# Kernel optimization log

Hardware: AMD Instinct MI355X
Metric: run time of the kernel (lower is better)

## Reference

```python
import jax, jax.numpy as jnp
import numpy as np

N_NODES = 100000
N_EDGES = 1600000
F_IN, F_HID, F_OUT = 48, 16, 16
K = 2  # kernel_size, dim=1, degree=1 open B-spline -> basis (1-u, u)


def glorot(key, shape):
    fan_in, fan_out = shape[-2], shape[-1]
    s = jnp.sqrt(6.0 / (fan_in + fan_out))
    return jax.random.uniform(key, shape, jnp.float32, -s, s)


def setup_inputs() -> dict:
    key = jax.random.key(0)
    ks = jax.random.split(key, 10)
    x = jax.random.normal(ks[0], (N_NODES, F_IN), jnp.float32)
    edge_attr = jax.random.uniform(ks[1], (N_EDGES, 1), jnp.float32)
    edge_index = jax.random.randint(ks[2], (2, N_EDGES), 0, N_NODES, jnp.int64)
    W1 = glorot(ks[3], (K, F_IN, F_HID))
    root1 = glorot(ks[4], (F_IN, F_HID))
    b1 = jnp.zeros((F_HID,), jnp.float32)
    W2 = glorot(ks[5], (K, F_HID, F_OUT))
    root2 = glorot(ks[6], (F_HID, F_OUT))
    b2 = jnp.zeros((F_OUT,), jnp.float32)
    return {"x": x, "edge_attr": edge_attr, "edge_index": edge_index,
            "W1": W1, "root1": root1, "b1": b1, "W2": W2, "root2": root2, "b2": b2}


def spline_conv(x, edge_index, u, W, root, bias, num_nodes):
    # x: [N,Fin], u: [E] pseudo coords in [0,1], W: [2,Fin,Fout]
    src, dst = edge_index[0], edge_index[1]
    xj = x[src]                                        # [E,Fin] gather
    m = jnp.einsum('ef,kfo->eko', xj, W)               # [E,2,Fout]
    basis = jnp.stack([1.0 - u, u], axis=1)            # linear open B-spline, K=2
    msg = jnp.einsum('ek,eko->eo', basis, m)           # [E,Fout]
    agg = jax.ops.segment_sum(msg, dst, num_segments=num_nodes)
    cnt = jax.ops.segment_sum(jnp.ones_like(msg[:, 0]), dst, num_segments=num_nodes)
    agg = agg / jnp.maximum(cnt, 1.0)[:, None]         # aggr='mean'
    return agg + x @ root + bias                       # root_weight + bias


def reference(x, edge_attr, edge_index, W1, root1, b1, W2, root2, b2):
    u = edge_attr[:, 0]
    h = jax.nn.elu(spline_conv(x, edge_index, u, W1, root1, b1, N_NODES))
    out = spline_conv(h, edge_index, u, W2, root2, b2, N_NODES)
    return jax.nn.log_softmax(out, axis=1)
```

## Files before the change

### kernel.cpp

```cpp
#include <hip/hip_runtime.h>
#include <math.h>

#define N_NODES 100000
#define N_EDGES 1600000
#define NBUK 782
#define BNODES 128
#define CAPSH 12
#define CAP 4096
#define NCHUNK 256
#define CPE 6250
#define NTBLK 1563
#define WS 52

#define NTL(p) __builtin_nontemporal_load(p)

__device__ __forceinline__ unsigned bf16_rne(float x) {
    unsigned u = __float_as_uint(x);
    return (u + 0x7FFFu + ((u >> 16) & 1u)) >> 16;
}

__device__ __forceinline__ void acc4(float* acc, uint4 w, float uu) {
    acc[0] += fmaf(uu, __uint_as_float(w.x & 0xFFFF0000u), __uint_as_float(w.x << 16));
    acc[1] += fmaf(uu, __uint_as_float(w.y & 0xFFFF0000u), __uint_as_float(w.y << 16));
    acc[2] += fmaf(uu, __uint_as_float(w.z & 0xFFFF0000u), __uint_as_float(w.z << 16));
    acc[3] += fmaf(uu, __uint_as_float(w.w & 0xFFFF0000u), __uint_as_float(w.w << 16));
}

__device__ __forceinline__ void edge_accum(unsigned pk,
                                           const uint4* __restrict__ YPH,
                                           float acc[16]) {
    float uu = (float)(pk >> 17) * (1.0f / 32767.0f);
    const uint4* yp = YPH + (size_t)(pk & 0x1FFFFu) * 4;
    uint4 w0 = yp[0], w1 = yp[1], w2 = yp[2], w3 = yp[3];
    acc4(acc + 0, w0, uu);
    acc4(acc + 4, w1, uu);
    acc4(acc + 8, w2, uu);
    acc4(acc + 12, w3, uu);
}

__device__ __forceinline__ void edge_accum2(unsigned p0, unsigned p1,
                                            const uint4* __restrict__ YPH,
                                            float acc[16]) {
    float u0 = (float)(p0 >> 17) * (1.0f / 32767.0f);
    float u1 = (float)(p1 >> 17) * (1.0f / 32767.0f);
    const uint4* a = YPH + (size_t)(p0 & 0x1FFFFu) * 4;
    const uint4* b = YPH + (size_t)(p1 & 0x1FFFFu) * 4;
    uint4 w0 = a[0], w1 = a[1], w2 = a[2], w3 = a[3];
    uint4 v0 = b[0], v1 = b[1], v2 = b[2], v3 = b[3];
    acc4(acc + 0, w0, u0);
    acc4(acc + 4, w1, u0);
    acc4(acc + 8, w2, u0);
    acc4(acc + 12, w3, u0);
    acc4(acc + 0, v0, u1);
    acc4(acc + 4, v1, u1);
    acc4(acc + 8, v2, u1);
    acc4(acc + 12, v3, u1);
}

__global__ __launch_bounds__(1024)
void transform1(const float* __restrict__ X,
                const float* __restrict__ W,
                const float* __restrict__ root,
                const float* __restrict__ bias,
                unsigned* __restrict__ YPH, float* __restrict__ R,
                int* __restrict__ cursor) {
    int t = threadIdx.x;
    if (blockIdx.x == NTBLK) {
        if (t < NBUK) cursor[t] = t * CAP;
        return;
    }
    __shared__ float sW0[16 * WS];
    __shared__ float sWd[16 * WS];
    __shared__ float sR[16 * WS];
    __shared__ float sB[16];
    for (int i = t; i < 48 * 16; i += 1024) {
        int f = i >> 4, o = i & 15;
        float w0 = W[i];
        float w1 = W[48 * 16 + i];
        sW0[o * WS + f] = w0;
        sWd[o * WS + f] = w1 - w0;
        sR[o * WS + f]  = root[i];
    }
    if (t < 16) sB[t] = bias[t];
    __syncthreads();

    int idx = blockIdx.x * 1024 + t;
    int n = idx >> 4;
    int o = idx & 15;
    if (n >= N_NODES) return;

    const float4* xr  = (const float4*)(X + (long)n * 48);
    const float4* w0p = (const float4*)(sW0 + o * WS);
    const float4* wdp = (const float4*)(sWd + o * WS);
    const float4* wrp = (const float4*)(sR  + o * WS);
    float a0 = 0.0f, a1 = 0.0f, ar = 0.0f;
#pragma unroll
    for (int fc = 0; fc < 12; ++fc) {
        float4 xv = xr[fc];
        float4 w0 = w0p[fc];
        float4 wd = wdp[fc];
        float4 wr = wrp[fc];
        a0 = fmaf(xv.x, w0.x, a0); a0 = fmaf(xv.y, w0.y, a0);
        a0 = fmaf(xv.z, w0.z, a0); a0 = fmaf(xv.w, w0.w, a0);
        a1 = fmaf(xv.x, wd.x, a1); a1 = fmaf(xv.y, wd.y, a1);
        a1 = fmaf(xv.z, wd.z, a1); a1 = fmaf(xv.w, wd.w, a1);
        ar = fmaf(xv.x, wr.x, ar); ar = fmaf(xv.y, wr.y, ar);
        ar = fmaf(xv.z, wr.z, ar); ar = fmaf(xv.w, wr.w, ar);
    }
    YPH[idx] = bf16_rne(a0) | (bf16_rne(a1) << 16);
    R[idx]   = ar + sB[o];
}

__global__ __launch_bounds__(1024)
void scatter_edges(const int* __restrict__ src, const int* __restrict__ dst,
                   const float* __restrict__ u,
                   int* __restrict__ cursor,
                   unsigned* __restrict__ pkb, unsigned char* __restrict__ dlb) {
    __shared__ unsigned upk[CPE];
    __shared__ unsigned short ubuk[CPE];
    __shared__ unsigned char udl[CPE];
    __shared__ unsigned spk[CPE];
    __shared__ unsigned char sdl[CPE];
    __shared__ unsigned short sbuk[CPE];
    __shared__ int lcur[NBUK];
    __shared__ int gbase[NBUK];
    __shared__ int sc[1024];

    int t = threadIdx.x, c = blockIdx.x;

    for (int i = t; i < NBUK; i += 1024) lcur[i] = 0;
    __syncthreads();
    for (int j = t; j < CPE; j += 1024) {
        int e = c * CPE + j;
        int d = NTL(dst + e);
        float uu = NTL(u + e);
        uu = uu < 0.0f ? 0.0f : (uu > 1.0f ? 1.0f : uu);
        int u15 = (int)fmaf(uu, 32767.0f, 0.5f);
        upk[j] = (unsigned)NTL(src + e) | ((unsigned)u15 << 17);
        udl[j] = (unsigned char)(d & 127);
        int b = d >> 7;
        ubuk[j] = (unsigned short)b;
        atomicAdd(&lcur[b], 1);
    }
    __syncthreads();

    int v = (t < NBUK) ? lcur[t] : 0;
    sc[t] = v;
    __syncthreads();
    for (int off = 1; off < 1024; off <<= 1) {
        int x = (t >= off) ? sc[t - off] : 0;
        __syncthreads();
        sc[t] += x;
        __syncthreads();
    }
    if (t < NBUK) {
        int ex = sc[t] - v;
        lcur[t] = ex;
        int base = atomicAdd(&cursor[t], v);
        gbase[t] = base - ex;
    }
    __syncthreads();

    for (int j = t; j < CPE; j += 1024) {
        int b = ubuk[j];
        int p = atomicAdd(&lcur[b], 1);
        spk[p] = upk[j];
        sdl[p] = udl[j];
        sbuk[p] = (unsigned short)b;
    }
    __syncthreads();

    for (int j = t; j < CPE; j += 1024) {
        int b = sbuk[j];
        int g = gbase[b] + j;
        if (g < ((b + 1) << CAPSH)) {
            pkb[g] = spk[j];
            dlb[g] = sdl[j];
        }
    }
}

__global__ __launch_bounds__(512)
void aggregate1(const int* __restrict__ cursor,
                const unsigned* __restrict__ pkb,
                const unsigned char* __restrict__ dlb,
                const uint4* __restrict__ YPH1,
                const float* __restrict__ R1,
                const float* __restrict__ W2,
                const float* __restrict__ root2,
                const float* __restrict__ b2,
                unsigned* __restrict__ YPH2,
                float* __restrict__ R2) {
    __shared__ unsigned spk[CAP];
    __shared__ int rp[BNODES + 1];
    __shared__ int cur[BNODES];
    __shared__ float sW0[256], sWd[256], sR[256], sB[16];
    int t = threadIdx.x, b = blockIdx.x;

    if (t < 256) {
        float w0 = W2[t], w1 = W2[256 + t];
        sW0[t] = w0;
        sWd[t] = w1 - w0;
        sR[t]  = root2[t];
    }
    if (t < 16) sB[t] = b2[t];
    if (t < BNODES) cur[t] = 0;
    __syncthreads();

    int cnt = cursor[b] - (b << CAPSH);
    if (cnt > CAP) cnt = CAP;
    const unsigned* pk = pkb + ((size_t)b << CAPSH);
    const unsigned char* dl = dlb + ((size_t)b << CAPSH);

    for (int j = t; j < cnt; j += 512) atomicAdd(&cur[NTL(dl + j)], 1);
    __syncthreads();

    int v = 0;
    if (t < BNODES) { v = cur[t]; rp[t] = v; }
    __syncthreads();
    for (int off = 1; off < BNODES; off <<= 1) {
        int x = 0;
        if (t < BNODES && t >= off) x = rp[t - off];
        __syncthreads();
        if (t < BNODES) rp[t] += x;
        __syncthreads();
    }
    if (t < BNODES) { int ex = rp[t] - v; rp[t] = ex; cur[t] = ex; }
    if (t == 0) rp[BNODES] = cnt;
    __syncthreads();

    for (int j = t; j < cnt; j += 512) {
        int d = NTL(dl + j);
        unsigned p = NTL(pk + j);
        int pos = atomicAdd(&cur[d], 1);
        spk[pos] = p;
    }
    __syncthreads();

    int node = t >> 2, q = t & 3;
    int n = (b << 7) + node;
    int beg = rp[node], end = rp[node + 1];
    int deg = end - beg;

    float acc[16];
#pragma unroll
    for (int i = 0; i < 16; ++i) acc[i] = 0.0f;
    int j = beg + q;
    for (; j + 4 < end; j += 8)
        edge_accum2(spk[j], spk[j + 4], YPH1, acc);
    if (j < end) edge_accum(spk[j], YPH1, acc);

#pragma unroll
    for (int mask = 1; mask <= 2; mask <<= 1) {
#pragma unroll
        for (int i = 0; i < 16; ++i) acc[i] += __shfl_xor(acc[i], mask);
    }

    if (n < N_NODES) {
        float inv = 1.0f / (deg > 0 ? (float)deg : 1.0f);
        float h16[16];
        const float4* rrp = (const float4*)(R1 + (size_t)n * 16);
#pragma unroll
        for (int qq = 0; qq < 4; ++qq) {
            float4 rr = rrp[qq];
            float w;
            w = fmaf(acc[4 * qq + 0], inv, rr.x); h16[4 * qq + 0] = w > 0.0f ? w : expm1f(w);
            w = fmaf(acc[4 * qq + 1], inv, rr.y); h16[4 * qq + 1] = w > 0.0f ? w : expm1f(w);
            w = fmaf(acc[4 * qq + 2], inv, rr.z); h16[4 * qq + 2] = w > 0.0f ? w : expm1f(w);
            w = fmaf(acc[4 * qq + 3], inv, rr.w); h16[4 * qq + 3] = w > 0.0f ? w : expm1f(w);
        }

        float a0[4] = {0, 0, 0, 0}, a1[4] = {0, 0, 0, 0}, ar[4] = {0, 0, 0, 0};
        int o0 = q * 4;
#pragma unroll
        for (int f = 0; f < 16; ++f) {
            float hv = h16[f];
#pragma unroll
            for (int o = 0; o < 4; ++o) {
                a0[o] = fmaf(hv, sW0[f * 16 + o0 + o], a0[o]);
                a1[o] = fmaf(hv, sWd[f * 16 + o0 + o], a1[o]);
                ar[o] = fmaf(hv, sR [f * 16 + o0 + o], ar[o]);
            }
        }
        uint4 yw;
        yw.x = bf16_rne(a0[0]) | (bf16_rne(a1[0]) << 16);
        yw.y = bf16_rne(a0[1]) | (bf16_rne(a1[1]) << 16);
        yw.z = bf16_rne(a0[2]) | (bf16_rne(a1[2]) << 16);
        yw.w = bf16_rne(a0[3]) | (bf16_rne(a1[3]) << 16);
        ((uint4*)YPH2)[(size_t)n * 4 + q] = yw;
        float4 rv;
        rv.x = ar[0] + sB[o0 + 0];
        rv.y = ar[1] + sB[o0 + 1];
        rv.z = ar[2] + sB[o0 + 2];
        rv.w = ar[3] + sB[o0 + 3];
        ((float4*)R2)[(size_t)n * 4 + q] = rv;
    }
}

__global__ __launch_bounds__(512)
void aggregate2(const int* __restrict__ cursor,
                const unsigned* __restrict__ pkb,
                const unsigned char* __restrict__ dlb,
                const uint4* __restrict__ YPH2,
                const float* __restrict__ R2,
                float* __restrict__ out) {
    __shared__ unsigned spk[CAP];
    __shared__ int rp[BNODES + 1];
    __shared__ int cur[BNODES];
    int t = threadIdx.x, b = blockIdx.x;

    if (t < BNODES) cur[t] = 0;
    __syncthreads();

    int cnt = cursor[b] - (b << CAPSH);
    if (cnt > CAP) cnt = CAP;
    const unsigned* pk = pkb + ((size_t)b << CAPSH);
    const unsigned char* dl = dlb + ((size_t)b << CAPSH);

    for (int j = t; j < cnt; j += 512) atomicAdd(&cur[NTL(dl + j)], 1);
    __syncthreads();

    int v = 0;
    if (t < BNODES) { v = cur[t]; rp[t] = v; }
    __syncthreads();
    for (int off = 1; off < BNODES; off <<= 1) {
        int x = 0;
        if (t < BNODES && t >= off) x = rp[t - off];
        __syncthreads();
        if (t < BNODES) rp[t] += x;
        __syncthreads();
    }
    if (t < BNODES) { int ex = rp[t] - v; rp[t] = ex; cur[t] = ex; }
    if (t == 0) rp[BNODES] = cnt;
    __syncthreads();

    for (int j = t; j < cnt; j += 512) {
        int d = NTL(dl + j);
        unsigned p = NTL(pk + j);
        int pos = atomicAdd(&cur[d], 1);
        spk[pos] = p;
    }
    __syncthreads();

    int node = t >> 2, q = t & 3;
    int n = (b << 7) + node;
    int beg = rp[node], end = rp[node + 1];
    int deg = end - beg;

    float acc[16];
#pragma unroll
    for (int i = 0; i < 16; ++i) acc[i] = 0.0f;
    int j = beg + q;
    for (; j + 4 < end; j += 8)
        edge_accum2(spk[j], spk[j + 4], YPH2, acc);
    if (j < end) edge_accum(spk[j], YPH2, acc);

#pragma unroll
    for (int mask = 1; mask <= 2; mask <<= 1) {
#pragma unroll
        for (int i = 0; i < 16; ++i) acc[i] += __shfl_xor(acc[i], mask);
    }

    if (n < N_NODES) {
        float inv = 1.0f / (deg > 0 ? (float)deg : 1.0f);
        float4 rr = ((const float4*)R2)[(size_t)n * 4 + q];
        float v0 = fmaf(acc[4 * q + 0], inv, rr.x);
        float v1 = fmaf(acc[4 * q + 1], inv, rr.y);
        float v2 = fmaf(acc[4 * q + 2], inv, rr.z);
        float v3 = fmaf(acc[4 * q + 3], inv, rr.w);
        float m = fmaxf(fmaxf(v0, v1), fmaxf(v2, v3));
        m = fmaxf(m, __shfl_xor(m, 1));
        m = fmaxf(m, __shfl_xor(m, 2));
        float s = expf(v0 - m) + expf(v1 - m) + expf(v2 - m) + expf(v3 - m);
        s += __shfl_xor(s, 1);
        s += __shfl_xor(s, 2);
        float lse = m + logf(s);
        float4 ov = make_float4(v0 - lse, v1 - lse, v2 - lse, v3 - lse);
        ((float4*)out)[(size_t)n * 4 + q] = ov;
    }
}

extern "C" void kernel_launch(void* const* d_in, const int* in_sizes, int n_in,
                              void* d_out, int out_size, void* d_ws, size_t ws_size,
                              hipStream_t stream) {
    const float* x         = (const float*)d_in[0];
    const float* edge_attr = (const float*)d_in[1];
    const int*   edge_idx  = (const int*)d_in[2];
    const float* W1        = (const float*)d_in[3];
    const float* root1     = (const float*)d_in[4];
    const float* b1        = (const float*)d_in[5];
    const float* W2        = (const float*)d_in[6];
    const float* root2     = (const float*)d_in[7];
    const float* b2        = (const float*)d_in[8];
    float* out = (float*)d_out;

    const int* src = edge_idx;
    const int* dst = edge_idx + N_EDGES;

    char* ws = (char*)d_ws;
    unsigned*      pkb    = (unsigned*)(ws);
    unsigned char* dlb    = (unsigned char*)(ws + 12812288);
    unsigned*      YPH1   = (unsigned*)(ws + 16015360);
    float*         R1     = (float*)(ws + 22415360);
    unsigned*      YPH2   = (unsigned*)(ws + 28815360);
    float*         R2     = (float*)(ws + 35215360);
    int*           cursor = (int*)(ws + 41615360);

    transform1<<<dim3(NTBLK + 1), 1024, 0, stream>>>(
        x, W1, root1, b1, YPH1, R1, cursor);

    scatter_edges<<<dim3(NCHUNK), 1024, 0, stream>>>(
        src, dst, edge_attr, cursor, pkb, dlb);

    aggregate1<<<dim3(NBUK), 512, 0, stream>>>(
        cursor, pkb, dlb, (const uint4*)YPH1, R1, W2, root2, b2, YPH2, R2);

    aggregate2<<<dim3(NBUK), 512, 0, stream>>>(
        cursor, pkb, dlb, (const uint4*)YPH2, R2, out);
}
```

Measured before the change: 189.2 us.

## Persist sorted edge order and row pointers from layer 1 for layer 2

```diff
diff --git a/kernel.cpp b/kernel.cpp
--- a/kernel.cpp
+++ b/kernel.cpp
@@ -7,10 +7,11 @@
 #define BNODES 128
 #define CAPSH 12
 #define CAP 4096
-#define NCHUNK 256
-#define CPE 6250
+#define NCHUNK 512
+#define CPE 3125
 #define NTBLK 1563
 #define WS 52
+#define RPW (BNODES + 1)
 
 #define NTL(p) __builtin_nontemporal_load(p)
 
@@ -182,8 +183,9 @@
 
 __global__ __launch_bounds__(512)
 void aggregate1(const int* __restrict__ cursor,
-                const unsigned* __restrict__ pkb,
+                unsigned* __restrict__ pkb,
                 const unsigned char* __restrict__ dlb,
+                int* __restrict__ rptab,
                 const uint4* __restrict__ YPH1,
                 const float* __restrict__ R1,
                 const float* __restrict__ W2,
@@ -192,7 +194,7 @@
                 unsigned* __restrict__ YPH2,
                 float* __restrict__ R2) {
     __shared__ unsigned spk[CAP];
-    __shared__ int rp[BNODES + 1];
+    __shared__ int rp[RPW];
     __shared__ int cur[BNODES];
     __shared__ float sW0[256], sWd[256], sR[256], sB[16];
     int t = threadIdx.x, b = blockIdx.x;
@@ -209,10 +211,18 @@
 
     int cnt = cursor[b] - (b << CAPSH);
     if (cnt > CAP) cnt = CAP;
-    const unsigned* pk = pkb + ((size_t)b << CAPSH);
+    unsigned* pk = pkb + ((size_t)b << CAPSH);
     const unsigned char* dl = dlb + ((size_t)b << CAPSH);
-
-    for (int j = t; j < cnt; j += 512) atomicAdd(&cur[NTL(dl + j)], 1);
+    int n4 = cnt >> 2, tail = cnt & 3, base4 = cnt & ~3;
+
+    for (int j4 = t; j4 < n4; j4 += 512) {
+        unsigned w = NTL((const unsigned*)dl + j4);
+        atomicAdd(&cur[w & 255], 1);
+        atomicAdd(&cur[(w >> 8) & 255], 1);
+        atomicAdd(&cur[(w >> 16) & 255], 1);
+        atomicAdd(&cur[w >> 24], 1);
+    }
+    if (t < tail) atomicAdd(&cur[NTL(dl + base4 + t)], 1);
     __syncthreads();
 
     int v = 0;
@@ -229,13 +239,22 @@
     if (t == 0) rp[BNODES] = cnt;
     __syncthreads();
 
-    for (int j = t; j < cnt; j += 512) {
-        int d = NTL(dl + j);
-        unsigned p = NTL(pk + j);
-        int pos = atomicAdd(&cur[d], 1);
-        spk[pos] = p;
-    }
-    __syncthreads();
+    for (int j4 = t; j4 < n4; j4 += 512) {
+        uint4 p = ((const uint4*)pk)[j4];
+        unsigned w = NTL((const unsigned*)dl + j4);
+        spk[atomicAdd(&cur[w & 255], 1)]         = p.x;
+        spk[atomicAdd(&cur[(w >> 8) & 255], 1)]  = p.y;
+        spk[atomicAdd(&cur[(w >> 16) & 255], 1)] = p.z;
+        spk[atomicAdd(&cur[w >> 24], 1)]         = p.w;
+    }
+    if (t < tail) {
+        int j = base4 + t;
+        spk[atomicAdd(&cur[NTL(dl + j)], 1)] = pk[j];
+    }
+    __syncthreads();
+
+    for (int j = t; j < cnt; j += 512) pk[j] = spk[j];
+    if (t < RPW) rptab[b * RPW + t] = rp[t];
 
     int node = t >> 2, q = t & 3;
     int n = (b << 7) + node;
@@ -298,50 +317,18 @@
 }
 
 __global__ __launch_bounds__(512)
-void aggregate2(const int* __restrict__ cursor,
+void aggregate2(const int* __restrict__ rptab,
                 const unsigned* __restrict__ pkb,
-                const unsigned char* __restrict__ dlb,
                 const uint4* __restrict__ YPH2,
                 const float* __restrict__ R2,
                 float* __restrict__ out) {
-    __shared__ unsigned spk[CAP];
-    __shared__ int rp[BNODES + 1];
-    __shared__ int cur[BNODES];
+    __shared__ int rp[RPW];
     int t = threadIdx.x, b = blockIdx.x;
 
-    if (t < BNODES) cur[t] = 0;
-    __syncthreads();
-
-    int cnt = cursor[b] - (b << CAPSH);
-    if (cnt > CAP) cnt = CAP;
+    if (t < RPW) rp[t] = rptab[b * RPW + t];
+    __syncthreads();
+
     const unsigned* pk = pkb + ((size_t)b << CAPSH);
-    const unsigned char* dl = dlb + ((size_t)b << CAPSH);
-
-    for (int j = t; j < cnt; j += 512) atomicAdd(&cur[NTL(dl + j)], 1);
-    __syncthreads();
-
-    int v = 0;
-    if (t < BNODES) { v = cur[t]; rp[t] = v; }
-    __syncthreads();
-    for (int off = 1; off < BNODES; off <<= 1) {
-        int x = 0;
-        if (t < BNODES && t >= off) x = rp[t - off];
-        __syncthreads();
-        if (t < BNODES) rp[t] += x;
-        __syncthreads();
-    }
-    if (t < BNODES) { int ex = rp[t] - v; rp[t] = ex; cur[t] = ex; }
-    if (t == 0) rp[BNODES] = cnt;
-    __syncthreads();
-
-    for (int j = t; j < cnt; j += 512) {
-        int d = NTL(dl + j);
-        unsigned p = NTL(pk + j);
-        int pos = atomicAdd(&cur[d], 1);
-        spk[pos] = p;
-    }
-    __syncthreads();
-
     int node = t >> 2, q = t & 3;
     int n = (b << 7) + node;
     int beg = rp[node], end = rp[node + 1];
@@ -352,8 +339,8 @@
     for (int i = 0; i < 16; ++i) acc[i] = 0.0f;
     int j = beg + q;
     for (; j + 4 < end; j += 8)
-        edge_accum2(spk[j], spk[j + 4], YPH2, acc);
-    if (j < end) edge_accum(spk[j], YPH2, acc);
+        edge_accum2(NTL(pk + j), NTL(pk + j + 4), YPH2, acc);
+    if (j < end) edge_accum(NTL(pk + j), YPH2, acc);
 
 #pragma unroll
     for (int mask = 1; mask <= 2; mask <<= 1) {
@@ -405,6 +392,7 @@
     unsigned*      YPH2   = (unsigned*)(ws + 28815360);
     float*         R2     = (float*)(ws + 35215360);
     int*           cursor = (int*)(ws + 41615360);
+    int*           rptab  = (int*)(ws + 41618496);
 
     transform1<<<dim3(NTBLK + 1), 1024, 0, stream>>>(
         x, W1, root1, b1, YPH1, R1, cursor);
@@ -413,8 +401,8 @@
         src, dst, edge_attr, cursor, pkb, dlb);
 
     aggregate1<<<dim3(NBUK), 512, 0, stream>>>(
-        cursor, pkb, dlb, (const uint4*)YPH1, R1, W2, root2, b2, YPH2, R2);
+        cursor, pkb, dlb, rptab, (const uint4*)YPH1, R1, W2, root2, b2, YPH2, R2);
 
     aggregate2<<<dim3(NBUK), 512, 0, stream>>>(
-        cursor, pkb, dlb, (const uint4*)YPH2, R2, out);
-}
+        rptab, pkb, (const uint4*)YPH2, R2, out);
+}
```

Measured after the change: 190.6 us. Within noise of the previous version (+0.7%).
